# Kernel tuning notes

Measured on AMD Instinct MI355X. Metric: run time of the kernel, lower is better.

The kernel has to match this reference:

```python
import jax, jax.numpy as jnp
import numpy as np

HH, WW = 7, 7  # pooled output size (module init: height, width)


def setup_inputs() -> dict:
    key = jax.random.key(0)
    k1, k2, k3, k4, k5 = jax.random.split(key, 5)
    C, Hf, Wf = 512, 64, 256        # conv feature map (stride 8)
    B = 4096                        # number of RoI boxes
    img_h, img_w = 512, 2048        # original image size
    feats = jax.random.normal(k1, (C, Hf, Wf), dtype=jnp.float32)
    w = jax.random.uniform(k2, (B,), minval=16.0, maxval=256.0)
    h = jax.random.uniform(k3, (B,), minval=16.0, maxval=128.0)
    xc = jax.random.uniform(k4, (B,), minval=0.0, maxval=float(img_w))
    yc = jax.random.uniform(k5, (B,), minval=0.0, maxval=float(img_h))
    boxes = jnp.stack([xc, yc, w, h], axis=1).astype(jnp.float32)  # (B,4) xc,yc,w,h in image coords
    return {"feats": feats, "boxes": boxes, "img_height": img_h, "img_width": img_w}


def _bilinear_sample(feats, px, py):
    """feats: (C,Hf,Wf); px,py: (B,HH,WW) pixel coords in feature map. Zero padding outside."""
    C, Hf, Wf = feats.shape
    x0 = jnp.floor(px)
    y0 = jnp.floor(py)
    x1 = x0 + 1.0
    y1 = y0 + 1.0
    wx1 = px - x0
    wx0 = 1.0 - wx1
    wy1 = py - y0
    wy0 = 1.0 - wy1

    def gather(xi, yi):
        valid = (xi >= 0) & (xi <= Wf - 1) & (yi >= 0) & (yi <= Hf - 1)
        xi_c = jnp.clip(xi, 0, Wf - 1).astype(jnp.int32)
        yi_c = jnp.clip(yi, 0, Hf - 1).astype(jnp.int32)
        v = feats[:, yi_c, xi_c]                     # (C,B,HH,WW)
        return v * valid[None].astype(feats.dtype)

    out = (gather(x0, y0) * (wx0 * wy0)[None]
           + gather(x1, y0) * (wx1 * wy0)[None]
           + gather(x0, y1) * (wx0 * wy1)[None]
           + gather(x1, y1) * (wx1 * wy1)[None])    # (C,B,HH,WW)
    return jnp.transpose(out, (1, 0, 2, 3))          # (B,C,HH,WW)


def reference(feats, boxes, img_height, img_width):
    # box_to_affine (densecap BoxToAffine, align_corners=True normalization) fused
    # with affine_grid: sample coords computed inline per box.
    B = boxes.shape[0]
    C, Hf, Wf = feats.shape
    xc, yc, w, h = boxes[:, 0], boxes[:, 1], boxes[:, 2], boxes[:, 3]
    tx = jnp.linspace(-1.0, 1.0, WW, dtype=feats.dtype)
    ty = jnp.linspace(-1.0, 1.0, HH, dtype=feats.dtype)
    inv_w = 1.0 / (img_width - 1)
    inv_h = 1.0 / (img_height - 1)
    # normalized image coords: gx = (2*xc-(W-1))/(W-1) + tx * w/(W-1)
    gx = (2.0 * xc[:, None] - (img_width - 1)) * inv_w + (w * inv_w)[:, None] * tx[None, :]   # (B,WW)
    gy = (2.0 * yc[:, None] - (img_height - 1)) * inv_h + (h * inv_h)[:, None] * ty[None, :]  # (B,HH)
    # map normalized [-1,1] to feature-map pixel coords (align_corners=True)
    px = (gx + 1.0) * 0.5 * (Wf - 1)
    py = (gy + 1.0) * 0.5 * (Hf - 1)
    px = jnp.broadcast_to(px[:, None, :], (B, HH, WW))
    py = jnp.broadcast_to(py[:, :, None], (B, HH, WW))
    return _bilinear_sample(feats, px, py)            # (B,C,HH,WW)
```

## Files before the change

kernel.cpp:

```cpp
#include <hip/hip_runtime.h>
#include <math.h>

#define HH 7
#define WW 7
#define CC 512
#define HF 64
#define WF 256
#define NS 49
#define CHUNK 64
#define ROWS4 (CC / 4)
#define NE4 ((CHUNK * NS) / 4)
#define NBINS 2048

typedef float floatv4 __attribute__((ext_vector_type(4)));

__global__ __launch_bounds__(256) void transpose_feats(const float* __restrict__ in,
                                                       float* __restrict__ out) {
    __shared__ float tile[32][33];
    const int P = HF * WF;
    int p  = blockIdx.x * 32 + threadIdx.x;
    int cb = blockIdx.y * 32;
#pragma unroll
    for (int r = 0; r < 32; r += 8)
        tile[threadIdx.y + r][threadIdx.x] = in[(size_t)(cb + threadIdx.y + r) * P + p];
    __syncthreads();
    int c  = cb + threadIdx.x;
    int pb = blockIdx.x * 32;
#pragma unroll
    for (int r = 0; r < 32; r += 8)
        out[(size_t)(pb + threadIdx.y + r) * CC + c] = tile[threadIdx.x][threadIdx.y + r];
}

__device__ __forceinline__ int box_key(const float* __restrict__ boxes, int b,
                                       float sy, float sx) {
    float xc = boxes[b * 4 + 0];
    float yc = boxes[b * 4 + 1];
    int yb = (int)(yc * sy);
    int xb = (int)(xc * sx);
    yb = min(max(yb, 0), 31);
    xb = min(max(xb, 0), 63);
    if (yb & 1) xb = 63 - xb;
    return (yb << 6) | xb;
}

__global__ __launch_bounds__(256) void hist_zero(int* __restrict__ hist) {
    hist[blockIdx.x * 256 + threadIdx.x] = 0;
}

__global__ __launch_bounds__(256) void hist_count(const float* __restrict__ boxes,
                                                  const int* __restrict__ ih_p,
                                                  const int* __restrict__ iw_p,
                                                  int B, int* __restrict__ hist) {
    int b = blockIdx.x * 256 + threadIdx.x;
    if (b < B) {
        float sy = 32.0f / (float)ih_p[0];
        float sx = 64.0f / (float)iw_p[0];
        atomicAdd(&hist[box_key(boxes, b, sy, sx)], 1);
    }
}

__global__ __launch_bounds__(256) void hist_scan(int* __restrict__ hist) {
    __shared__ int part[256];
    const int tid  = threadIdx.x;
    const int base = tid * (NBINS / 256);
    int v[NBINS / 256];
    int s = 0;
#pragma unroll
    for (int i = 0; i < NBINS / 256; ++i) { v[i] = s; s += hist[base + i]; }
    part[tid] = s;
    __syncthreads();
    for (int d = 1; d < 256; d <<= 1) {
        int t = (tid >= d) ? part[tid - d] : 0;
        __syncthreads();
        part[tid] += t;
        __syncthreads();
    }
    const int off = part[tid] - s;
#pragma unroll
    for (int i = 0; i < NBINS / 256; ++i) hist[base + i] = v[i] + off;
}

__global__ __launch_bounds__(256) void scatter_perm(const float* __restrict__ boxes,
                                                    const int* __restrict__ ih_p,
                                                    const int* __restrict__ iw_p,
                                                    int B, int* __restrict__ hist,
                                                    int* __restrict__ perm) {
    int b = blockIdx.x * 256 + threadIdx.x;
    if (b < B) {
        float sy = 32.0f / (float)ih_p[0];
        float sx = 64.0f / (float)iw_p[0];
        int pos = atomicAdd(&hist[box_key(boxes, b, sy, sx)], 1);
        perm[pos] = b;
    }
}

__device__ __forceinline__ void box_setup(int s, int b,
                                          const float* __restrict__ boxes,
                                          const int* __restrict__ ih_p,
                                          const int* __restrict__ iw_p,
                                          int4* o_out, float4* w_out) {
    int i = s / WW;
    int j = s - i * WW;
    float IW1 = (float)(iw_p[0] - 1);
    float IH1 = (float)(ih_p[0] - 1);
    float xc = boxes[b * 4 + 0];
    float yc = boxes[b * 4 + 1];
    float bw = boxes[b * 4 + 2];
    float bh = boxes[b * 4 + 3];
    float inv_w = 1.0f / IW1;
    float inv_h = 1.0f / IH1;
    float tx = (float)(j - 3) * (1.0f / 3.0f);
    float ty = (float)(i - 3) * (1.0f / 3.0f);
    float gx = (2.0f * xc - IW1) * inv_w + (bw * inv_w) * tx;
    float gy = (2.0f * yc - IH1) * inv_h + (bh * inv_h) * ty;
    float px = (gx + 1.0f) * 0.5f * (float)(WF - 1);
    float py = (gy + 1.0f) * 0.5f * (float)(HF - 1);

    float x0f = floorf(px), y0f = floorf(py);
    float wx1 = px - x0f, wx0 = 1.0f - wx1;
    float wy1 = py - y0f, wy0 = 1.0f - wy1;
    float x1f = x0f + 1.0f, y1f = y0f + 1.0f;

    bool vx0 = (x0f >= 0.0f) && (x0f <= (float)(WF - 1));
    bool vx1 = (x1f >= 0.0f) && (x1f <= (float)(WF - 1));
    bool vy0 = (y0f >= 0.0f) && (y0f <= (float)(HF - 1));
    bool vy1 = (y1f >= 0.0f) && (y1f <= (float)(HF - 1));

    int xi0 = (int)fminf(fmaxf(x0f, 0.0f), (float)(WF - 1));
    int xi1 = (int)fminf(fmaxf(x1f, 0.0f), (float)(WF - 1));
    int yi0 = (int)fminf(fmaxf(y0f, 0.0f), (float)(HF - 1));
    int yi1 = (int)fminf(fmaxf(y1f, 0.0f), (float)(HF - 1));

    int4 o;
    o.x = yi0 * WF + xi0;
    o.y = yi0 * WF + xi1;
    o.z = yi1 * WF + xi0;
    o.w = yi1 * WF + xi1;
    float4 w4;
    w4.x = wx0 * wy0 * ((vx0 && vy0) ? 1.0f : 0.0f);
    w4.y = wx1 * wy0 * ((vx1 && vy0) ? 1.0f : 0.0f);
    w4.z = wx0 * wy1 * ((vx0 && vy1) ? 1.0f : 0.0f);
    w4.w = wx1 * wy1 * ((vx1 && vy1) ? 1.0f : 0.0f);
    *o_out = o;
    *w_out = w4;
}

__global__ __launch_bounds__(256) void roi_pool_v7(const float* __restrict__ src,
                                                   const float* __restrict__ boxes,
                                                   const int* __restrict__ ih_p,
                                                   const int* __restrict__ iw_p,
                                                   const int* __restrict__ perm,
                                                   float* __restrict__ out) {
    __shared__ int4   s_off[NS];
    __shared__ float4 s_wt[NS];
    __shared__ float  tile[CHUNK * 64];

    const int nwg  = gridDim.x;
    const int bid  = blockIdx.x;
    const int q    = nwg >> 3, r = nwg & 7;
    const int xcd  = bid & 7, slot = bid >> 3;
    const int rank = xcd * q + min(xcd, r) + slot;
    const int b    = perm[rank];

    const int tid = threadIdx.x;
    const int g   = tid & 15;
    const int ph  = tid >> 4;

    if (tid < NS) {
        int4 o; float4 w4;
        box_setup(tid, b, boxes, ih_p, iw_p, &o, &w4);
        o.x *= ROWS4; o.y *= ROWS4; o.z *= ROWS4; o.w *= ROWS4;
        s_off[tid] = o;
        s_wt[tid]  = w4;
    }
    __syncthreads();

    int4   o_r[4];
    float4 w_r[4];
    int    sig_r[4];
#pragma unroll
    for (int it = 0; it < 4; ++it) {
        int s = ph + (it << 4);
        if (s < NS) {
            o_r[it]   = s_off[s];
            w_r[it]   = s_wt[s];
            sig_r[it] = (s >> 2) | ((s & 3) << 4);
        }
    }

    const size_t outbase = (size_t)b * (CC * NS);
    const float4* src4   = (const float4*)src;

    for (int c0 = 0; c0 < CC; c0 += CHUNK) {
        const int cb4 = c0 >> 2;
#pragma unroll
        for (int it = 0; it < 4; ++it) {
            int s = ph + (it << 4);
            if (s < NS) {
                int4   o = o_r[it];
                float4 w = w_r[it];
                float4 a  = src4[o.x + cb4 + g];
                float4 bb = src4[o.y + cb4 + g];
                float4 c  = src4[o.z + cb4 + g];
                float4 d  = src4[o.w + cb4 + g];
                int base = g << 8;
                int sw   = sig_r[it] ^ g;
                tile[base +       sw] = a.x * w.x + bb.x * w.y + c.x * w.z + d.x * w.w;
                tile[base +  64 + sw] = a.y * w.x + bb.y * w.y + c.y * w.z + d.y * w.w;
                tile[base + 128 + sw] = a.z * w.x + bb.z * w.y + c.z * w.z + d.z * w.w;
                tile[base + 192 + sw] = a.w * w.x + bb.w * w.y + c.w * w.z + d.w * w.w;
            }
        }
        __syncthreads();
        float* outc = out + outbase + (size_t)c0 * NS;
        for (int k4 = tid; k4 < NE4; k4 += 256) {
            int e = k4 << 2;
            int c = e / NS;
            int s = e - c * NS;
            floatv4 v;
            v.x = tile[(c << 6) + (((s >> 2) | ((s & 3) << 4)) ^ (c >> 2))];
            if (++s == NS) { s = 0; ++c; }
            v.y = tile[(c << 6) + (((s >> 2) | ((s & 3) << 4)) ^ (c >> 2))];
            if (++s == NS) { s = 0; ++c; }
            v.z = tile[(c << 6) + (((s >> 2) | ((s & 3) << 4)) ^ (c >> 2))];
            if (++s == NS) { s = 0; ++c; }
            v.w = tile[(c << 6) + (((s >> 2) | ((s & 3) << 4)) ^ (c >> 2))];
            __builtin_nontemporal_store(v, (floatv4*)outc + k4);
        }
        __syncthreads();
    }
}

__global__ __launch_bounds__(256) void roi_pool_fb(const float* __restrict__ src,
                                                   const float* __restrict__ boxes,
                                                   const int* __restrict__ ih_p,
                                                   const int* __restrict__ iw_p,
                                                   float* __restrict__ out) {
    __shared__ int4   s_off[NS];
    __shared__ float4 s_wt[NS];
    __shared__ float  tile[NS * 257];

    const int b   = blockIdx.x;
    const int tid = threadIdx.x;

    if (tid < NS) {
        int4 o; float4 w4;
        box_setup(tid, b, boxes, ih_p, iw_p, &o, &w4);
        s_off[tid] = o;
        s_wt[tid]  = w4;
    }
    __syncthreads();

    const size_t outbase = (size_t)b * (CC * NS);
    for (int c0 = 0; c0 < CC; c0 += 256) {
        const int cterm = (c0 + tid) * (HF * WF);
        for (int s = 0; s < NS; ++s) {
            int4   o = s_off[s];
            float4 w = s_wt[s];
            float v = src[o.x + cterm] * w.x + src[o.y + cterm] * w.y +
                      src[o.z + cterm] * w.z + src[o.w + cterm] * w.w;
            tile[s * 257 + tid] = v;
        }
        __syncthreads();
        const size_t ob = outbase + (size_t)c0 * NS;
        for (int k = tid; k < 256 * NS; k += 256) {
            int cl = k / NS;
            int s  = k - cl * NS;
            out[ob + k] = tile[s * 257 + cl];
        }
        __syncthreads();
    }
}

extern "C" void kernel_launch(void* const* d_in, const int* in_sizes, int n_in,
                              void* d_out, int out_size, void* d_ws, size_t ws_size,
                              hipStream_t stream) {
    const float* feats = (const float*)d_in[0];
    const float* boxes = (const float*)d_in[1];
    const int*   ih    = (const int*)d_in[2];
    const int*   iw    = (const int*)d_in[3];
    float*       out   = (float*)d_out;
    const int B = in_sizes[1] / 4;

    const size_t tf_bytes = (size_t)CC * HF * WF * sizeof(float);
    const size_t need = tf_bytes + (size_t)B * sizeof(int) + (size_t)NBINS * sizeof(int);
    if (ws_size >= need) {
        float* tf   = (float*)d_ws;
        int*   perm = (int*)((char*)d_ws + tf_bytes);
        int*   hist = (int*)((char*)d_ws + tf_bytes + (size_t)B * sizeof(int));
        dim3 tb(32, 8);
        dim3 tg((HF * WF) / 32, CC / 32);
        transpose_feats<<<tg, tb, 0, stream>>>(feats, tf);
        hist_zero<<<NBINS / 256, 256, 0, stream>>>(hist);
        hist_count<<<(B + 255) / 256, 256, 0, stream>>>(boxes, ih, iw, B, hist);
        hist_scan<<<1, 256, 0, stream>>>(hist);
        scatter_perm<<<(B + 255) / 256, 256, 0, stream>>>(boxes, ih, iw, B, hist, perm);
        roi_pool_v7<<<B, 256, 0, stream>>>(tf, boxes, ih, iw, perm, out);
    } else {
        roi_pool_fb<<<B, 256, 0, stream>>>(feats, boxes, ih, iw, out);
    }
}
```

Baseline: 464.5 us.

## Double-buffer LDS tile to overlap gathers with output stores in RoI pool

Splits the per-chunk loop into load, compute-to-LDS and write-out phases and uses two LDS tiles. The gathers for chunk cc are issued before the write-out of chunk cc-1, and one barrier per iteration replaces two. The aim is to hide gather latency behind the output stores, at the cost of doubled LDS use (32KB) and more live registers, which may reduce occupancy.

Result: slower. 474.2 us (+2.1%).

```diff
diff --git a/kernel.cpp b/kernel.cpp
--- a/kernel.cpp
+++ b/kernel.cpp
@@ -8,6 +8,7 @@
 #define WF 256
 #define NS 49
 #define CHUNK 64
+#define NCHUNK (CC / CHUNK)
 #define ROWS4 (CC / 4)
 #define NE4 ((CHUNK * NS) / 4)
 #define NBINS 2048
@@ -145,7 +146,7 @@
     *w_out = w4;
 }
 
-__global__ __launch_bounds__(256) void roi_pool_v7(const float* __restrict__ src,
+__global__ __launch_bounds__(256) void roi_pool_v8(const float* __restrict__ src,
                                                    const float* __restrict__ boxes,
                                                    const int* __restrict__ ih_p,
                                                    const int* __restrict__ iw_p,
@@ -153,7 +154,7 @@
                                                    float* __restrict__ out) {
     __shared__ int4   s_off[NS];
     __shared__ float4 s_wt[NS];
-    __shared__ float  tile[CHUNK * 64];
+    __shared__ float  tile[2][CHUNK * 64];
 
     const int nwg  = gridDim.x;
     const int bid  = blockIdx.x;
@@ -191,44 +192,77 @@
     const size_t outbase = (size_t)b * (CC * NS);
     const float4* src4   = (const float4*)src;
 
-    for (int c0 = 0; c0 < CC; c0 += CHUNK) {
-        const int cb4 = c0 >> 2;
-#pragma unroll
-        for (int it = 0; it < 4; ++it) {
-            int s = ph + (it << 4);
-            if (s < NS) {
-                int4   o = o_r[it];
-                float4 w = w_r[it];
-                float4 a  = src4[o.x + cb4 + g];
-                float4 bb = src4[o.y + cb4 + g];
-                float4 c  = src4[o.z + cb4 + g];
-                float4 d  = src4[o.w + cb4 + g];
-                int base = g << 8;
-                int sw   = sig_r[it] ^ g;
-                tile[base +       sw] = a.x * w.x + bb.x * w.y + c.x * w.z + d.x * w.w;
-                tile[base +  64 + sw] = a.y * w.x + bb.y * w.y + c.y * w.z + d.y * w.w;
-                tile[base + 128 + sw] = a.z * w.x + bb.z * w.y + c.z * w.z + d.z * w.w;
-                tile[base + 192 + sw] = a.w * w.x + bb.w * w.y + c.w * w.z + d.w * w.w;
-            }
-        }
-        __syncthreads();
-        float* outc = out + outbase + (size_t)c0 * NS;
-        for (int k4 = tid; k4 < NE4; k4 += 256) {
-            int e = k4 << 2;
-            int c = e / NS;
-            int s = e - c * NS;
-            floatv4 v;
-            v.x = tile[(c << 6) + (((s >> 2) | ((s & 3) << 4)) ^ (c >> 2))];
-            if (++s == NS) { s = 0; ++c; }
-            v.y = tile[(c << 6) + (((s >> 2) | ((s & 3) << 4)) ^ (c >> 2))];
-            if (++s == NS) { s = 0; ++c; }
-            v.z = tile[(c << 6) + (((s >> 2) | ((s & 3) << 4)) ^ (c >> 2))];
-            if (++s == NS) { s = 0; ++c; }
-            v.w = tile[(c << 6) + (((s >> 2) | ((s & 3) << 4)) ^ (c >> 2))];
-            __builtin_nontemporal_store(v, (floatv4*)outc + k4);
-        }
-        __syncthreads();
-    }
+    float4 A_[4], B_[4], C_[4], D_[4];
+
+#define LOADS(cc_)                                                          \
+    do {                                                                    \
+        const int cb4_ = (cc_) << 4;                                        \
+        _Pragma("unroll")                                                   \
+        for (int it = 0; it < 4; ++it) {                                    \
+            int s_ = ph + (it << 4);                                        \
+            if (s_ < NS) {                                                  \
+                int4 o_ = o_r[it];                                          \
+                A_[it] = src4[o_.x + cb4_ + g];                             \
+                B_[it] = src4[o_.y + cb4_ + g];                             \
+                C_[it] = src4[o_.z + cb4_ + g];                             \
+                D_[it] = src4[o_.w + cb4_ + g];                             \
+            }                                                               \
+        }                                                                   \
+    } while (0)
+
+#define FMAST(buf_)                                                         \
+    do {                                                                    \
+        float* tb_ = &tile[buf_][0];                                        \
+        _Pragma("unroll")                                                   \
+        for (int it = 0; it < 4; ++it) {                                    \
+            int s_ = ph + (it << 4);                                        \
+            if (s_ < NS) {                                                  \
+                float4 w_ = w_r[it];                                        \
+                int base_ = g << 8;                                         \
+                int sw_   = sig_r[it] ^ g;                                  \
+                tb_[base_ +       sw_] = A_[it].x * w_.x + B_[it].x * w_.y + C_[it].x * w_.z + D_[it].x * w_.w; \
+                tb_[base_ +  64 + sw_] = A_[it].y * w_.x + B_[it].y * w_.y + C_[it].y * w_.z + D_[it].y * w_.w; \
+                tb_[base_ + 128 + sw_] = A_[it].z * w_.x + B_[it].z * w_.y + C_[it].z * w_.z + D_[it].z * w_.w; \
+                tb_[base_ + 192 + sw_] = A_[it].w * w_.x + B_[it].w * w_.y + C_[it].w * w_.z + D_[it].w * w_.w; \
+            }                                                               \
+        }                                                                   \
+    } while (0)
+
+#define WRITEPH(cc_, buf_)                                                  \
+    do {                                                                    \
+        const float* tb_ = &tile[buf_][0];                                  \
+        float* outc_ = out + outbase + (size_t)((cc_) * CHUNK) * NS;        \
+        for (int k4 = tid; k4 < NE4; k4 += 256) {                           \
+            int e_ = k4 << 2;                                               \
+            int c_ = e_ / NS;                                               \
+            int s_ = e_ - c_ * NS;                                          \
+            floatv4 v_;                                                     \
+            v_.x = tb_[(c_ << 6) + (((s_ >> 2) | ((s_ & 3) << 4)) ^ (c_ >> 2))]; \
+            if (++s_ == NS) { s_ = 0; ++c_; }                               \
+            v_.y = tb_[(c_ << 6) + (((s_ >> 2) | ((s_ & 3) << 4)) ^ (c_ >> 2))]; \
+            if (++s_ == NS) { s_ = 0; ++c_; }                               \
+            v_.z = tb_[(c_ << 6) + (((s_ >> 2) | ((s_ & 3) << 4)) ^ (c_ >> 2))]; \
+            if (++s_ == NS) { s_ = 0; ++c_; }                               \
+            v_.w = tb_[(c_ << 6) + (((s_ >> 2) | ((s_ & 3) << 4)) ^ (c_ >> 2))]; \
+            __builtin_nontemporal_store(v_, (floatv4*)outc_ + k4);          \
+        }                                                                   \
+    } while (0)
+
+    LOADS(0);
+    FMAST(0);
+    __syncthreads();
+
+    for (int cc = 1; cc < NCHUNK; ++cc) {
+        LOADS(cc);
+        WRITEPH(cc - 1, (cc - 1) & 1);
+        FMAST(cc & 1);
+        __syncthreads();
+    }
+    WRITEPH(NCHUNK - 1, (NCHUNK - 1) & 1);
+
+#undef LOADS
+#undef FMAST
+#undef WRITEPH
 }
 
 __global__ __launch_bounds__(256) void roi_pool_fb(const float* __restrict__ src,
@@ -295,7 +329,7 @@
         hist_count<<<(B + 255) / 256, 256, 0, stream>>>(boxes, ih, iw, B, hist);
         hist_scan<<<1, 256, 0, stream>>>(hist);
         scatter_perm<<<(B + 255) / 256, 256, 0, stream>>>(boxes, ih, iw, B, hist, perm);
-        roi_pool_v7<<<B, 256, 0, stream>>>(tf, boxes, ih, iw, perm, out);
+        roi_pool_v8<<<B, 256, 0, stream>>>(tf, boxes, ih, iw, perm, out);
     } else {
         roi_pool_fb<<<B, 256, 0, stream>>>(feats, boxes, ih, iw, out);
     }
```

## Split each RoI across channel slices into separate workgroups

Applied to the files above, without the earlier changes.

Each box is now handled by eight workgroups, one per 64-channel slice, instead of one workgroup looping over all eight slices. This launches eight times as many blocks to raise parallelism and latency hiding, and it removes the per-slice barriers within a block. In exchange, the per-box setup (box_setup, perm lookup) is repeated eight times. The XCD-aware mapping is rewritten so that one XCD's consecutive blocks walk through its boxes for each slice in turn, with a simple fallback when B is not a multiple of 8.

Result: no change. 455.5 us (-1.9%).

```diff
diff --git a/kernel.cpp b/kernel.cpp
--- a/kernel.cpp
+++ b/kernel.cpp
@@ -8,6 +8,7 @@
 #define WF 256
 #define NS 49
 #define CHUNK 64
+#define NSLICE (CC / CHUNK)
 #define ROWS4 (CC / 4)
 #define NE4 ((CHUNK * NS) / 4)
 #define NBINS 2048
@@ -145,22 +146,30 @@
     *w_out = w4;
 }
 
-__global__ __launch_bounds__(256) void roi_pool_v7(const float* __restrict__ src,
-                                                   const float* __restrict__ boxes,
-                                                   const int* __restrict__ ih_p,
-                                                   const int* __restrict__ iw_p,
-                                                   const int* __restrict__ perm,
-                                                   float* __restrict__ out) {
+__global__ __launch_bounds__(256) void roi_pool_v10(const float* __restrict__ src,
+                                                    const float* __restrict__ boxes,
+                                                    const int* __restrict__ ih_p,
+                                                    const int* __restrict__ iw_p,
+                                                    const int* __restrict__ perm,
+                                                    int B,
+                                                    float* __restrict__ out) {
     __shared__ int4   s_off[NS];
     __shared__ float4 s_wt[NS];
     __shared__ float  tile[CHUNK * 64];
 
-    const int nwg  = gridDim.x;
-    const int bid  = blockIdx.x;
-    const int q    = nwg >> 3, r = nwg & 7;
-    const int xcd  = bid & 7, slot = bid >> 3;
-    const int rank = xcd * q + min(xcd, r) + slot;
-    const int b    = perm[rank];
+    const int bid = blockIdx.x;
+    int slice, rank;
+    if ((B & 7) == 0) {
+        const int xcd = bid & 7;
+        const int seq = bid >> 3;
+        const int per = B >> 3;
+        slice = seq / per;
+        rank  = xcd * per + (seq - slice * per);
+    } else {
+        slice = bid % NSLICE;
+        rank  = bid / NSLICE;
+    }
+    const int b = perm[rank];
 
     const int tid = threadIdx.x;
     const int g   = tid & 15;
@@ -175,59 +184,45 @@
     }
     __syncthreads();
 
-    int4   o_r[4];
-    float4 w_r[4];
-    int    sig_r[4];
+    const size_t outbase = (size_t)b * (CC * NS);
+    const float4* src4   = (const float4*)src;
+    const int cb4        = slice << 4;
+
 #pragma unroll
     for (int it = 0; it < 4; ++it) {
         int s = ph + (it << 4);
         if (s < NS) {
-            o_r[it]   = s_off[s];
-            w_r[it]   = s_wt[s];
-            sig_r[it] = (s >> 2) | ((s & 3) << 4);
+            int4   o = s_off[s];
+            float4 w = s_wt[s];
+            float4 a  = src4[o.x + cb4 + g];
+            float4 bb = src4[o.y + cb4 + g];
+            float4 c  = src4[o.z + cb4 + g];
+            float4 d  = src4[o.w + cb4 + g];
+            int base = g << 8;
+            int sig  = (s >> 2) | ((s & 3) << 4);
+            int sw   = sig ^ g;
+            tile[base +       sw] = a.x * w.x + bb.x * w.y + c.x * w.z + d.x * w.w;
+            tile[base +  64 + sw] = a.y * w.x + bb.y * w.y + c.y * w.z + d.y * w.w;
+            tile[base + 128 + sw] = a.z * w.x + bb.z * w.y + c.z * w.z + d.z * w.w;
+            tile[base + 192 + sw] = a.w * w.x + bb.w * w.y + c.w * w.z + d.w * w.w;
         }
     }
-
-    const size_t outbase = (size_t)b * (CC * NS);
-    const float4* src4   = (const float4*)src;
-
-    for (int c0 = 0; c0 < CC; c0 += CHUNK) {
-        const int cb4 = c0 >> 2;
-#pragma unroll
-        for (int it = 0; it < 4; ++it) {
-            int s = ph + (it << 4);
-            if (s < NS) {
-                int4   o = o_r[it];
-                float4 w = w_r[it];
-                float4 a  = src4[o.x + cb4 + g];
-                float4 bb = src4[o.y + cb4 + g];
-                float4 c  = src4[o.z + cb4 + g];
-                float4 d  = src4[o.w + cb4 + g];
-                int base = g << 8;
-                int sw   = sig_r[it] ^ g;
-                tile[base +       sw] = a.x * w.x + bb.x * w.y + c.x * w.z + d.x * w.w;
-                tile[base +  64 + sw] = a.y * w.x + bb.y * w.y + c.y * w.z + d.y * w.w;
-                tile[base + 128 + sw] = a.z * w.x + bb.z * w.y + c.z * w.z + d.z * w.w;
-                tile[base + 192 + sw] = a.w * w.x + bb.w * w.y + c.w * w.z + d.w * w.w;
-            }
-        }
-        __syncthreads();
-        float* outc = out + outbase + (size_t)c0 * NS;
-        for (int k4 = tid; k4 < NE4; k4 += 256) {
-            int e = k4 << 2;
-            int c = e / NS;
-            int s = e - c * NS;
-            floatv4 v;
-            v.x = tile[(c << 6) + (((s >> 2) | ((s & 3) << 4)) ^ (c >> 2))];
-            if (++s == NS) { s = 0; ++c; }
-            v.y = tile[(c << 6) + (((s >> 2) | ((s & 3) << 4)) ^ (c >> 2))];
-            if (++s == NS) { s = 0; ++c; }
-            v.z = tile[(c << 6) + (((s >> 2) | ((s & 3) << 4)) ^ (c >> 2))];
-            if (++s == NS) { s = 0; ++c; }
-            v.w = tile[(c << 6) + (((s >> 2) | ((s & 3) << 4)) ^ (c >> 2))];
-            __builtin_nontemporal_store(v, (floatv4*)outc + k4);
-        }
-        __syncthreads();
+    __syncthreads();
+
+    float* outc = out + outbase + (size_t)(slice * CHUNK) * NS;
+    for (int k4 = tid; k4 < NE4; k4 += 256) {
+        int e = k4 << 2;
+        int c = e / NS;
+        int s = e - c * NS;
+        floatv4 v;
+        v.x = tile[(c << 6) + (((s >> 2) | ((s & 3) << 4)) ^ (c >> 2))];
+        if (++s == NS) { s = 0; ++c; }
+        v.y = tile[(c << 6) + (((s >> 2) | ((s & 3) << 4)) ^ (c >> 2))];
+        if (++s == NS) { s = 0; ++c; }
+        v.z = tile[(c << 6) + (((s >> 2) | ((s & 3) << 4)) ^ (c >> 2))];
+        if (++s == NS) { s = 0; ++c; }
+        v.w = tile[(c << 6) + (((s >> 2) | ((s & 3) << 4)) ^ (c >> 2))];
+        __builtin_nontemporal_store(v, (floatv4*)outc + k4);
     }
 }
 
@@ -295,7 +290,7 @@
         hist_count<<<(B + 255) / 256, 256, 0, stream>>>(boxes, ih, iw, B, hist);
         hist_scan<<<1, 256, 0, stream>>>(hist);
         scatter_perm<<<(B + 255) / 256, 256, 0, stream>>>(boxes, ih, iw, B, hist, perm);
-        roi_pool_v7<<<B, 256, 0, stream>>>(tf, boxes, ih, iw, perm, out);
+        roi_pool_v10<<<NSLICE * B, 256, 0, stream>>>(tf, boxes, ih, iw, perm, B, out);
     } else {
         roi_pool_fb<<<B, 256, 0, stream>>>(feats, boxes, ih, iw, out);
     }
```
